# Optimization experiments

Measured on AMD Instinct MI355X. Metric: run time of the kernel, lower is better.

## Reference

```python
import jax, jax.numpy as jnp
import numpy as np

B, C, H, W = 8, 256, 96, 96
NQ, NCLS = 100, 12
OBJ_CH = NCLS - 2 + 1  # 11
EPS = 1e-6


def conv2d(x, w, b, pad):
    out = jax.lax.conv_general_dilated(x, w, (1, 1), [(pad, pad), (pad, pad)],
                                       dimension_numbers=('NCHW', 'OIHW', 'NCHW'))
    return out + b[None, :, None, None]


def conv1d(x, w, b):
    out = jax.lax.conv_general_dilated(x, w, (1,), [(0, 0)],
                                       dimension_numbers=('NCH', 'OIH', 'NCH'))
    return out + b[None, :, None]


def adaptive_avg_pool_1d(x, out_size):
    # x: [..., L]; torch AdaptiveAvgPool semantics: bin i = mean(x[floor(i*L/o):ceil((i+1)*L/o)])
    L = x.shape[-1]
    i = np.arange(out_size)
    starts = (i * L) // out_size
    ends = -((-(i + 1) * L) // out_size)
    csum = jnp.concatenate([jnp.zeros(x.shape[:-1] + (1,), x.dtype), jnp.cumsum(x, -1)], -1)
    sizes = jnp.asarray((ends - starts).astype(np.float32))
    return (csum[..., ends] - csum[..., starts]) / sizes


def local_max(p):
    # 8-neighbor local maximum with zero padding, thresholded at EPS
    pd = jnp.pad(p, ((0, 0), (0, 0), (1, 1), (1, 1)))
    m = ((p >= pd[:, :, :-2, 1:-1]) & (p >= pd[:, :, 2:, 1:-1]) &
         (p >= pd[:, :, 1:-1, :-2]) & (p >= pd[:, :, 1:-1, 2:]) &
         (p >= pd[:, :, :-2, :-2]) & (p >= pd[:, :, :-2, 2:]) &
         (p >= pd[:, :, 2:, :-2]) & (p >= pd[:, :, 2:, 2:]) & (p >= EPS))
    return m.astype(p.dtype)


def mask_and_nms(probs):
    # one-hot mask from argmax over foreground channels, then add local-max map
    oh = jax.nn.one_hot(jnp.argmax(probs[:, :-1], axis=1), probs.shape[1], axis=1, dtype=probs.dtype)
    p = probs * oh
    return p + local_max(p)


def head(x, w1, b1, w2, b2):
    return conv2d(jax.nn.relu(conv2d(x, w1, b1, 1)), w2, b2, 0)


def setup_inputs() -> dict:
    key = jax.random.key(0)
    ks = jax.random.split(key, 20)
    rn = lambda k, s: jax.random.normal(k, s, jnp.float32) * 0.02
    z = lambda n: jnp.zeros((n,), jnp.float32)
    return {
        'x': jax.random.normal(ks[0], (B, C, H, W), jnp.float32),
        'y': jax.random.normal(ks[1], (B, C, H, W), jnp.float32),
        'pos_embeddings': jax.random.normal(ks[2], (1, C, H, W), jnp.float32),
        'lw1': rn(ks[3], (C, C, 3, 3)), 'lb1': z(C),
        'lw2': rn(ks[4], (2, C, 1, 1)), 'lb2': z(2),
        'rw1': rn(ks[5], (C, C, 3, 3)), 'rb1': z(C),
        'rw2': rn(ks[6], (2, C, 1, 1)), 'rb2': z(2),
        'ow1': rn(ks[7], (C, C, 3, 3)), 'ob1': z(C),
        'ow2': rn(ks[8], (OBJ_CH, C, 1, 1)), 'ob2': z(OBJ_CH),
        'cw1': rn(ks[9], (64, C, 3, 3)), 'cb1': z(64),
        'cw2': rn(ks[10], (32, 64, 3, 3)), 'cb2': z(32),
        'cm_lw': rn(ks[11], (778 * 2, 778 * 32)), 'cm_lb': z(778 * 2),
        'c1d_w': rn(ks[12], (C, 2, 3)), 'c1d_b': z(C),
        'q_lw': rn(ks[13], (NQ * C, C)), 'q_lb': z(NQ * C),
    }


def reference(x, y, pos_embeddings, lw1, lb1, lw2, lb2, rw1, rb1, rw2, rb2,
              ow1, ob1, ow2, ob2, cw1, cb1, cw2, cb2, cm_lw, cm_lb,
              c1d_w, c1d_b, q_lw, q_lb):
    b = x.shape[0]
    left_logits = head(x, lw1, lb1, lw2, lb2)
    right_logits = head(x, rw1, rb1, rw2, rb2)
    obj_logits = head(x, ow1, ob1, ow2, ob2)

    left_p = mask_and_nms(jax.nn.softmax(left_logits, axis=1))
    right_p = mask_and_nms(jax.nn.softmax(right_logits, axis=1))
    obj_p = mask_and_nms(jax.nn.softmax(obj_logits, axis=1))

    hw = H * W
    idx_l = jax.lax.top_k(left_p[:, 0].reshape(b, hw), 40)[1]
    idx_r = jax.lax.top_k(right_p[:, 0].reshape(b, hw), 40)[1]
    idx_o = jax.lax.top_k(obj_p[:, :-1].reshape(b, OBJ_CH - 1, hw).max(axis=1), 20)[1]
    idx = jnp.concatenate([idx_l, idx_r, idx_o], axis=1)  # [B, 100]

    xf = x.reshape(b, C, hw)
    topk_proposals = jnp.take_along_axis(xf, jnp.broadcast_to(idx[:, None, :], (b, C, NQ)), axis=2)
    pf = jnp.broadcast_to(pos_embeddings, (b, C, H, W)).reshape(b, C, hw)
    topk_pos = jnp.take_along_axis(pf, jnp.broadcast_to(idx[:, None, :], (b, C, NQ)), axis=2)

    # contact map estimation branch
    h = jax.nn.relu(conv2d(y, cw1, cb1, 1))
    h = jax.nn.relu(conv2d(h, cw2, cb2, 1))  # [B,32,H,W]
    h = jnp.mean(h, axis=3)                  # adaptive pool width -> 1
    h = adaptive_avg_pool_1d(h, 778)         # [B,32,778]
    cm = h.reshape(b, -1) @ cm_lw.T + cm_lb  # [B,1556]
    contact_map = cm.reshape(b, 2, 778, 1)

    # ContactMapConvolution
    cc = conv1d(contact_map.reshape(b, 2, 778), c1d_w, c1d_b)  # [B,C,776]
    cc = jnp.mean(cc, axis=2)                                  # [B,C]
    feat = (cc @ q_lw.T + q_lb).reshape(b, C, NQ)              # [B,C,100]

    topk_proposals = topk_proposals + feat
    return (topk_proposals, topk_pos, left_logits, right_logits, obj_logits, contact_map)
```

## Files before the change

### kernel.cpp

```cpp
#include <hip/hip_runtime.h>
#include <float.h>
#include <math.h>

#define B_ 8
#define C_ 256
#define H_ 96
#define W_ 96
#define HW_ 9216
#define NQ_ 100
#define EPS_ 1e-6f
#define PADW_ 98
#define PADIMG_ 9604
#define PALLOC_ 76880

typedef unsigned short ushort_t;
typedef __attribute__((ext_vector_type(8))) short bf16x8;
typedef __attribute__((ext_vector_type(16))) float f32x16;

typedef __attribute__((address_space(3))) unsigned int as3_u32;
typedef __attribute__((address_space(1))) unsigned int as1_u32;

__device__ __forceinline__ void gl16(const void* g, void* l) {
    __builtin_amdgcn_global_load_lds(
        (const as1_u32*)(unsigned long long)g,
        (as3_u32*)(unsigned int)(unsigned long long)l, 16, 0, 0);
}

__device__ __forceinline__ ushort_t bf16_of(float v) {
    unsigned u = __float_as_uint(v);
    u += 0x7fffu + ((u >> 16) & 1u);
    return (ushort_t)(u >> 16);
}
__device__ __forceinline__ float f_of_bf16(ushort_t h) {
    return __uint_as_float((unsigned)h << 16);
}

__global__ __launch_bounds__(256)
void zero_border_kernel(ushort_t* __restrict__ bh, ushort_t* __restrict__ bl, int Cch)
{
    int per = 388 * Cch / 8;
    int id = blockIdx.x * 256 + threadIdx.x;
    if (id >= 8 * per) return;
    int b = id / per, i = id - b * per;
    int pi = (i * 8) / Cch, c8 = (i * 8) % Cch;
    int yy, xx;
    if (pi < 98)      { yy = 0;            xx = pi; }
    else if (pi < 196){ yy = 97;           xx = pi - 98; }
    else if (pi < 292){ yy = pi - 195;     xx = 0; }
    else              { yy = pi - 291;     xx = 97; }
    size_t base = ((size_t)b * PADIMG_ + yy * PADW_ + xx) * Cch + c8;
    *(bf16x8*)&bh[base] = (bf16x8)(short)0;
    *(bf16x8*)&bl[base] = (bf16x8)(short)0;
}

__global__ __launch_bounds__(256)
void tsplit_kernel(const float* __restrict__ in, ushort_t* __restrict__ oh,
                   ushort_t* __restrict__ ol, int Cch)
{
    __shared__ float T[32][33];
    const int tx = threadIdx.x & 31, ty = threadIdx.x >> 5;
    const int p0 = blockIdx.x * 32, ci0 = blockIdx.y * 32, b = blockIdx.z;
#pragma unroll
    for (int i = 0; i < 4; ++i)
        T[ty + 8*i][tx] = in[((size_t)b*Cch + ci0 + ty + 8*i)*HW_ + p0 + tx];
    __syncthreads();
    const int y = p0 / 96, x0 = p0 - y * 96;
    const size_t Pp = (size_t)b*PADIMG_ + (size_t)(y + 1)*PADW_ + x0 + 1;
#pragma unroll
    for (int i = 0; i < 4; ++i) {
        float v = T[tx][ty + 8*i];
        ushort_t hi = bf16_of(v);
        float lo = v - f_of_bf16(hi);
        size_t o = (Pp + ty + 8*i)*Cch + ci0 + tx;
        oh[o] = hi;
        ol[o] = bf16_of(lo);
    }
}

__global__ __launch_bounds__(256)
void repack_kernel(const float* __restrict__ w, ushort_t* __restrict__ wh,
                   ushort_t* __restrict__ wl, int Cout, int Cin)
{
    int id = blockIdx.x*256 + threadIdx.x;
    int tot = 9*Cout*Cin;
    if (id >= tot) return;
    int tap = id / (Cout*Cin);
    int r = id - tap*(Cout*Cin);
    int oc = r / Cin, ci = r - oc*Cin;
    float v = w[((size_t)oc*Cin + ci)*9 + tap];
    ushort_t hi = bf16_of(v);
    wh[id] = hi;
    wl[id] = bf16_of(v - f_of_bf16(hi));
}

template<int WM, int WN, int MFR, int NFR, int CIN, int MODE, int KK, int BWAVES>
__global__ __launch_bounds__(WM*WN*64, (WM*WN + 3) / 4)
void conv_gemm_kernel(const ushort_t* __restrict__ Agh, const ushort_t* __restrict__ Agl,
                      const ushort_t* __restrict__ Wgh, const ushort_t* __restrict__ Wgl,
                      const float* __restrict__ bias1,
                      const float* __restrict__ w2, const float* __restrict__ b2,
                      float* __restrict__ out_logits,
                      ushort_t* __restrict__ Oth, ushort_t* __restrict__ Otl,
                      float* __restrict__ outf)
{
    constexpr int NW    = WM*WN;
    constexpr int NT    = NW*64;
    constexpr int BM    = WM*MFR*32;
    constexpr int COUT  = WN*NFR*32;
    constexpr int NG    = CIN/16;
    constexpr int NSTEP = NG*9;
    constexpr int APAD  = 512;
    constexpr int ASZ   = 2*APAD*16;
    constexpr int BSZ   = 2*COUT*16;
    constexpr int AROUNDS = 32;
    constexpr int BROUNDS = COUT/16;
    constexpr int AWAVES = NW - BWAVES;
    constexpr int AR_PER = AROUNDS/AWAVES;
    constexpr int BR_PER = BROUNDS/BWAVES;
    static_assert(BM == 288, "BM must be 288");
    static_assert(AROUNDS % AWAVES == 0, "");
    static_assert(BROUNDS % BWAVES == 0, "");

    __shared__ __align__(16) ushort_t ALds[2*ASZ];
    __shared__ __align__(16) ushort_t BLds[3*BSZ];

    const int tid  = threadIdx.x;
    const int lane = tid & 63;
    const int wid  = __builtin_amdgcn_readfirstlane(tid >> 6);
    const int wm   = wid / WN, wn = wid % WN;
    const int l31  = lane & 31, hh2 = lane >> 5;
    const int wnb  = wn * NFR * 32;

    const int cpx = gridDim.x >> 3;
    const int bid = (blockIdx.x & 7)*cpx + (blockIdx.x >> 3);
    const int bidx = bid >> 5;
    const int br   = bid & 31;
    const size_t S = (size_t)bidx*PADIMG_ + (size_t)(3*br)*PADW_;

    auto stageA = [&](int g, int sel) {
        ushort_t* dst = ALds + sel*ASZ;
        const int aw = wid - BWAVES;
#pragma unroll
        for (int j = 0; j < AR_PER; ++j) {
            int c = aw*AR_PER + j;
            int id = c*64 + lane;
            int split = id >> 10;
            int r2 = id & 1023;
            int pix = r2 >> 1, ch = r2 & 1;
            int ch2 = ch ^ (pix & 1);
            const ushort_t* src = (split ? Agl : Agh) + (S + pix)*CIN + g*16 + ch2*8;
            gl16(src, dst + (size_t)c*512);
        }
    };
    auto stageB = [&](int g, int tap, int sel) {
        ushort_t* dst = BLds + sel*BSZ;
#pragma unroll
        for (int j = 0; j < BR_PER; ++j) {
            int c = wid*BR_PER + j;
            int id = c*64 + lane;
            int split = id / (COUT*2);
            int r2 = id % (COUT*2);
            int row = r2 >> 1, ch = r2 & 1;
            int ch2 = ch ^ (row & 1);
            const ushort_t* src = (split ? Wgl : Wgh)
                + ((size_t)tap*COUT + row)*CIN + g*16 + ch2*8;
            gl16(src, dst + (size_t)c*512);
        }
    };

    f32x16 acc[MFR][NFR];
#pragma unroll
    for (int i = 0; i < MFR; ++i)
#pragma unroll
        for (int j = 0; j < NFR; ++j)
#pragma unroll
            for (int r = 0; r < 16; ++r) acc[i][j][r] = 0.f;

    if (wid < BWAVES) { stageB(0, 0, 0); stageB(0, 1, 1); }
    else stageA(0, 0);
    asm volatile("s_waitcnt vmcnt(0)" ::: "memory");
    __builtin_amdgcn_s_barrier();
    __builtin_amdgcn_sched_barrier(0);

    int g = 0, tap = 0;
#pragma unroll 1
    for (int step = 0; step < NSTEP; ++step) {
        __builtin_amdgcn_sched_barrier(0);
        if (wid < BWAVES) {
            if (step >= NSTEP - 1) asm volatile("s_waitcnt vmcnt(0)" ::: "memory");
            else                   asm volatile("s_waitcnt vmcnt(%0)" :: "n"(BR_PER) : "memory");
        } else if (tap == 0) {
            asm volatile("s_waitcnt vmcnt(0)" ::: "memory");
        }
        __builtin_amdgcn_s_barrier();
        __builtin_amdgcn_sched_barrier(0);

        if (wid < BWAVES) {
            if (step + 2 < NSTEP) {
                int t2 = tap + 2, g2 = g;
                if (t2 >= 9) { t2 -= 9; ++g2; }
                stageB(g2, t2, (step + 2) % 3);
            }
        } else if (tap == 0 && g + 1 < NG) {
            stageA(g + 1, (g + 1) & 1);
        }

        const int abase = (g & 1) * ASZ;
        const int bbase = (step % 3) * BSZ;
        const int dy = tap / 3, dx = tap - dy*3;
        const int tapoff = dy*PADW_ + dx;

        bf16x8 bh[NFR], bl[NFR];
#pragma unroll
        for (int nf = 0; nf < NFR; ++nf) {
            int n = wnb + nf*32 + l31;
            int o = bbase + n*16 + ((hh2 ^ (n & 1)) << 3);
            bh[nf] = *(const bf16x8*)&BLds[o];
            bl[nf] = *(const bf16x8*)&BLds[o + COUT*16];
        }
        __builtin_amdgcn_s_setprio(1);
#pragma unroll
        for (int mf = 0; mf < MFR; ++mf) {
            int row = wm*PADW_ + tapoff + mf*32 + l31;
            int o = abase + row*16 + ((hh2 ^ (row & 1)) << 3);
            bf16x8 ah = *(const bf16x8*)&ALds[o];
            bf16x8 al = *(const bf16x8*)&ALds[o + APAD*16];
#pragma unroll
            for (int nf = 0; nf < NFR; ++nf) {
                acc[mf][nf] = __builtin_amdgcn_mfma_f32_32x32x16_bf16(
                    ah, bh[nf], acc[mf][nf], 0, 0, 0);
                acc[mf][nf] = __builtin_amdgcn_mfma_f32_32x32x16_bf16(
                    al, bh[nf], acc[mf][nf], 0, 0, 0);
                acc[mf][nf] = __builtin_amdgcn_mfma_f32_32x32x16_bf16(
                    ah, bl[nf], acc[mf][nf], 0, 0, 0);
            }
        }
        __builtin_amdgcn_s_setprio(0);

        if (++tap == 9) { tap = 0; ++g; }
    }
    __syncthreads();

    float biasv[NFR];
#pragma unroll
    for (int nf = 0; nf < NFR; ++nf) biasv[nf] = bias1[wnb + nf*32 + l31];

    if constexpr (MODE == 0) {
        float* Lacc = (float*)ALds;
        float w2v[NFR][KK];
#pragma unroll
        for (int nf = 0; nf < NFR; ++nf)
#pragma unroll
            for (int k = 0; k < KK; ++k)
                w2v[nf][k] = w2[(size_t)k*COUT + wnb + nf*32 + l31];

#pragma unroll
        for (int mf = 0; mf < MFR; ++mf) {
#pragma unroll
            for (int r = 0; r < 16; ++r) {
                float v[KK];
#pragma unroll
                for (int k = 0; k < KK; ++k) v[k] = 0.f;
#pragma unroll
                for (int nf = 0; nf < NFR; ++nf) {
                    float rr = fmaxf(acc[mf][nf][r] + biasv[nf], 0.f);
#pragma unroll
                    for (int k = 0; k < KK; ++k) v[k] += rr * w2v[nf][k];
                }
#pragma unroll
                for (int k = 0; k < KK; ++k) {
                    v[k] += __shfl_xor(v[k], 1);
                    v[k] += __shfl_xor(v[k], 2);
                    v[k] += __shfl_xor(v[k], 4);
                    v[k] += __shfl_xor(v[k], 8);
                    v[k] += __shfl_xor(v[k], 16);
                }
                if (l31 == 0) {
                    int crow = (r & 3) + 8*(r >> 2) + 4*hh2;
                    int mrow = wm*96 + mf*32 + crow;
#pragma unroll
                    for (int k = 0; k < KK; ++k)
                        Lacc[((size_t)wn*BM + mrow)*KK + k] = v[k];
                }
            }
        }
        __syncthreads();
        for (int i = tid; i < BM*KK; i += NT) {
            int mrow = i / KK, k = i - mrow*KK;
            float s = b2[k];
#pragma unroll
            for (int w = 0; w < WN; ++w) s += Lacc[((size_t)w*BM + mrow)*KK + k];
            out_logits[((size_t)bidx*KK + k)*HW_ + br*288 + mrow] = s;
        }
    } else if constexpr (MODE == 1) {
#pragma unroll
        for (int mf = 0; mf < MFR; ++mf)
#pragma unroll
            for (int nf = 0; nf < NFR; ++nf)
#pragma unroll
                for (int r = 0; r < 16; ++r) {
                    float rr = fmaxf(acc[mf][nf][r] + biasv[nf], 0.f);
                    ushort_t hi = bf16_of(rr);
                    float lo = rr - f_of_bf16(hi);
                    int crow = (r & 3) + 8*(r >> 2) + 4*hh2;
                    int xx = mf*32 + crow;
                    size_t Pp = (size_t)bidx*PADIMG_
                              + (size_t)(3*br + wm + 1)*PADW_ + xx + 1;
                    size_t o = Pp*COUT + wnb + nf*32 + l31;
                    Oth[o] = hi;
                    Otl[o] = bf16_of(lo);
                }
    } else {
        float (*T)[BM + 1] = (float(*)[BM + 1])ALds;
#pragma unroll
        for (int mf = 0; mf < MFR; ++mf)
#pragma unroll
            for (int r = 0; r < 16; ++r) {
                float rr = fmaxf(acc[mf][0][r] + biasv[0], 0.f);
                int crow = (r & 3) + 8*(r >> 2) + 4*hh2;
                T[l31][wm*96 + mf*32 + crow] = rr;
            }
        __syncthreads();
        for (int i = tid; i < COUT*BM; i += NT) {
            int c = i / BM, m = i - c*BM;
            outf[((size_t)bidx*COUT + c)*HW_ + br*288 + m] = T[c][m];
        }
    }
}

__global__ __launch_bounds__(256)
void prob2_kernel(const float* __restrict__ logits, float* __restrict__ p0)
{
    int i = blockIdx.x * 256 + threadIdx.x;
    if (i >= B_ * HW_) return;
    int b = i / HW_, pix = i - b * HW_;
    float l0 = logits[(size_t)b * 2 * HW_ + pix];
    float l1 = logits[(size_t)b * 2 * HW_ + HW_ + pix];
    float m = fmaxf(l0, l1);
    float e0 = expf(l0 - m), e1 = expf(l1 - m);
    p0[i] = e0 / (e0 + e1);
}

__global__ __launch_bounds__(256)
void score2_kernel(const float* __restrict__ p, float* __restrict__ sc)
{
    int i = blockIdx.x * 256 + threadIdx.x;
    if (i >= B_ * HW_) return;
    int pix = i % HW_;
    int yy = pix / W_, xx = pix - (pix / W_) * W_;
    float c = p[i];
    bool ok = (c >= EPS_);
    const float* pb = p + (i - pix);
#pragma unroll
    for (int dy = -1; dy <= 1; ++dy)
#pragma unroll
        for (int dx = -1; dx <= 1; ++dx) {
            if (dy == 0 && dx == 0) continue;
            int ny = yy + dy, nx = xx + dx;
            float v = 0.f;
            if (ny >= 0 && ny < H_ && nx >= 0 && nx < W_) v = pb[ny * W_ + nx];
            ok = ok && (c >= v);
        }
    sc[i] = c + (ok ? 1.f : 0.f);
}

__global__ __launch_bounds__(256)
void probobj_kernel(const float* __restrict__ logits, float* __restrict__ pval,
                    int* __restrict__ cstar)
{
    int i = blockIdx.x * 256 + threadIdx.x;
    if (i >= B_ * HW_) return;
    int b = i / HW_, pix = i - b * HW_;
    const float* lb = logits + (size_t)b * 11 * HW_ + pix;
    float l[11];
#pragma unroll
    for (int c2 = 0; c2 < 11; ++c2) l[c2] = lb[(size_t)c2 * HW_];
    float m = l[0];
#pragma unroll
    for (int c2 = 1; c2 < 11; ++c2) m = fmaxf(m, l[c2]);
    float sum = 0.f;
#pragma unroll
    for (int c2 = 0; c2 < 11; ++c2) sum += expf(l[c2] - m);
    int a = 0; float bestl = l[0];
#pragma unroll
    for (int c2 = 1; c2 < 10; ++c2)
        if (l[c2] > bestl) { bestl = l[c2]; a = c2; }
    pval[i] = expf(bestl - m) / sum;
    cstar[i] = a;
}

__global__ __launch_bounds__(256)
void score11_kernel(const float* __restrict__ p, const int* __restrict__ cs,
                    float* __restrict__ sc)
{
    int i = blockIdx.x * 256 + threadIdx.x;
    if (i >= B_ * HW_) return;
    int pix = i % HW_;
    int yy = pix / W_, xx = pix - (pix / W_) * W_;
    float c = p[i];
    int cc = cs[i];
    bool ok = (c >= EPS_);
    int base = i - pix;
#pragma unroll
    for (int dy = -1; dy <= 1; ++dy)
#pragma unroll
        for (int dx = -1; dx <= 1; ++dx) {
            if (dy == 0 && dx == 0) continue;
            int ny = yy + dy, nx = xx + dx;
            float v = 0.f;
            if (ny >= 0 && ny < H_ && nx >= 0 && nx < W_) {
                int n = base + ny * W_ + nx;
                v = (cs[n] == cc) ? p[n] : 0.f;
            }
            ok = ok && (c >= v);
        }
    sc[i] = c + (ok ? 1.f : 0.f);
}

__global__ __launch_bounds__(256)
void topk_kernel(const float* __restrict__ scL, const float* __restrict__ scR,
                 const float* __restrict__ scO, int* __restrict__ idx)
{
    __shared__ float sv[HW_];
    __shared__ float rv[256];
    __shared__ int   ri[256];
    const int h = blockIdx.x, b = blockIdx.y;
    const float* src = (h == 0) ? scL : (h == 1) ? scR : scO;
    const int k = (h == 2) ? 20 : 40;
    const int off = b * NQ_ + ((h == 0) ? 0 : (h == 1) ? 40 : 80);

    for (int t = threadIdx.x; t < HW_; t += 256) sv[t] = src[(size_t)b * HW_ + t];
    __syncthreads();

    for (int kk = 0; kk < k; ++kk) {
        float bestv = -FLT_MAX; int besti = HW_;
        for (int t = threadIdx.x; t < HW_; t += 256) {
            float v = sv[t];
            if (v > bestv) { bestv = v; besti = t; }
        }
        rv[threadIdx.x] = bestv; ri[threadIdx.x] = besti;
        __syncthreads();
        for (int s = 128; s > 0; s >>= 1) {
            if (threadIdx.x < s) {
                float v2 = rv[threadIdx.x + s]; int i2 = ri[threadIdx.x + s];
                if (v2 > rv[threadIdx.x] ||
                    (v2 == rv[threadIdx.x] && i2 < ri[threadIdx.x])) {
                    rv[threadIdx.x] = v2; ri[threadIdx.x] = i2;
                }
            }
            __syncthreads();
        }
        if (threadIdx.x == 0) { idx[off + kk] = ri[0]; sv[ri[0]] = -FLT_MAX; }
        __syncthreads();
    }
}

__global__ __launch_bounds__(128)
void pool_kernel(const float* __restrict__ h2, float* __restrict__ pooled)
{
    int bc = blockIdx.x;
    __shared__ float row[96];
    for (int hh = threadIdx.x; hh < 96; hh += 128) {
        const float* p = h2 + (size_t)bc * HW_ + hh * W_;
        float s = 0.f;
        for (int ww = 0; ww < 96; ++ww) s += p[ww];
        row[hh] = s * (1.f / 96.f);
    }
    __syncthreads();
    for (int i = threadIdx.x; i < 778; i += 128) {
        int s0 = (i * 96) / 778;
        int e0 = ((i + 1) * 96 + 777) / 778;
        float s = 0.f;
        for (int t = s0; t < e0; ++t) s += row[t];
        pooled[(size_t)bc * 778 + i] = s / (float)(e0 - s0);
    }
}

__global__ __launch_bounds__(256)
void cm_kernel(const float* __restrict__ pooled, const float* __restrict__ cm_lw,
               const float* __restrict__ cm_lb, float* __restrict__ out5)
{
    const int j = blockIdx.x;
    const float* wr = cm_lw + (size_t)j * 24896;
    float acc[8];
#pragma unroll
    for (int b = 0; b < 8; ++b) acc[b] = 0.f;
    for (int t = threadIdx.x; t < 24896; t += 256) {
        float w = wr[t];
#pragma unroll
        for (int b = 0; b < 8; ++b) acc[b] += w * pooled[(size_t)b * 24896 + t];
    }
    __shared__ float red[8][256];
#pragma unroll
    for (int b = 0; b < 8; ++b) red[b][threadIdx.x] = acc[b];
    __syncthreads();
    for (int s = 128; s > 0; s >>= 1) {
        if (threadIdx.x < s) {
#pragma unroll
            for (int b = 0; b < 8; ++b) red[b][threadIdx.x] += red[b][threadIdx.x + s];
        }
        __syncthreads();
    }
    if (threadIdx.x < 8)
        out5[(size_t)threadIdx.x * 1556 + j] = red[threadIdx.x][0] + cm_lb[j];
}

__global__ __launch_bounds__(256)
void c1d_kernel(const float* __restrict__ cmap, const float* __restrict__ w,
                const float* __restrict__ bias, float* __restrict__ ccmean)
{
    int b = blockIdx.x;
    __shared__ float r[2][778];
    __shared__ float T[2][3];
    for (int t = threadIdx.x; t < 1556; t += 256)
        r[t / 778][t % 778] = cmap[(size_t)b * 1556 + t];
    __syncthreads();
    if (threadIdx.x < 2) {
        int ic = threadIdx.x;
        float s = 0.f;
        for (int i2 = 0; i2 < 778; ++i2) s += r[ic][i2];
        T[ic][0] = s - r[ic][776] - r[ic][777];
        T[ic][1] = s - r[ic][0]   - r[ic][777];
        T[ic][2] = s - r[ic][0]   - r[ic][1];
    }
    __syncthreads();
    int oc = threadIdx.x;
    float a = 0.f;
#pragma unroll
    for (int ic = 0; ic < 2; ++ic)
#pragma unroll
        for (int k = 0; k < 3; ++k)
            a += w[oc * 6 + ic * 3 + k] * T[ic][k];
    ccmean[b * 256 + oc] = a / 776.f + bias[oc];
}

__global__ __launch_bounds__(256)
void feat_kernel(const float* __restrict__ ccmean, const float* __restrict__ q_lw,
                 const float* __restrict__ q_lb, float* __restrict__ feat)
{
    __shared__ float cc[8][256];
    for (int t = threadIdx.x; t < 2048; t += 256) cc[t >> 8][t & 255] = ccmean[t];
    __syncthreads();
    int j = blockIdx.x * 256 + threadIdx.x;
    const float* wr = q_lw + (size_t)j * 256;
    float acc[8];
#pragma unroll
    for (int b = 0; b < 8; ++b) acc[b] = 0.f;
    for (int c = 0; c < 256; ++c) {
        float wv = wr[c];
#pragma unroll
        for (int b = 0; b < 8; ++b) acc[b] += wv * cc[b][c];
    }
    float qb = q_lb[j];
#pragma unroll
    for (int b = 0; b < 8; ++b) feat[(size_t)b * 25600 + j] = acc[b] + qb;
}

__global__ __launch_bounds__(256)
void gather_kernel(const float* __restrict__ x, const float* __restrict__ pos,
                   const float* __restrict__ feat, const int* __restrict__ idx,
                   float* __restrict__ out0, float* __restrict__ out1)
{
    int t = blockIdx.x * 256 + threadIdx.x;
    if (t >= B_ * C_ * NQ_) return;
    int q = t % NQ_;
    int c2 = (t / NQ_) % C_;
    int b = t / (C_ * NQ_);
    int p = idx[b * NQ_ + q];
    out0[t] = x[((size_t)b * C_ + c2) * HW_ + p] + feat[(size_t)b * 25600 + c2 * NQ_ + q];
    out1[t] = pos[(size_t)c2 * HW_ + p];
}

extern "C" void kernel_launch(void* const* d_in, const int* in_sizes, int n_in,
                              void* d_out, int out_size, void* d_ws, size_t ws_size,
                              hipStream_t stream) {
    const float* x    = (const float*)d_in[0];
    const float* y    = (const float*)d_in[1];
    const float* pos  = (const float*)d_in[2];
    const float* lw1  = (const float*)d_in[3];  const float* lb1 = (const float*)d_in[4];
    const float* lw2  = (const float*)d_in[5];  const float* lb2 = (const float*)d_in[6];
    const float* rw1  = (const float*)d_in[7];  const float* rb1 = (const float*)d_in[8];
    const float* rw2  = (const float*)d_in[9];  const float* rb2 = (const float*)d_in[10];
    const float* ow1  = (const float*)d_in[11]; const float* ob1 = (const float*)d_in[12];
    const float* ow2  = (const float*)d_in[13]; const float* ob2 = (const float*)d_in[14];
    const float* cw1  = (const float*)d_in[15]; const float* cb1 = (const float*)d_in[16];
    const float* cw2  = (const float*)d_in[17]; const float* cb2 = (const float*)d_in[18];
    const float* cmlw = (const float*)d_in[19]; const float* cmlb = (const float*)d_in[20];
    const float* c1dw = (const float*)d_in[21]; const float* c1db = (const float*)d_in[22];
    const float* qlw  = (const float*)d_in[23]; const float* qlb  = (const float*)d_in[24];

    float* out  = (float*)d_out;
    float* out0 = out;
    float* out1 = out + 204800;
    float* out2 = out + 409600;
    float* out3 = out + 557056;
    float* out4 = out + 704512;
    float* out5 = out + 1515520;

    float* ws = (float*)d_ws;
    ushort_t* Rh   = (ushort_t*)(ws);
    ushort_t* Rl   = (ushort_t*)(ws + 9840640);
    ushort_t* h1h  = (ushort_t*)(ws + 19681280);
    ushort_t* h1l  = (ushort_t*)(ws + 22141440);
    float*    h2   = ws + 24601600;
    ushort_t* wLh  = (ushort_t*)(ws + 26960896);
    ushort_t* wLl  = (ushort_t*)(ws + 27255808);
    ushort_t* wRh  = (ushort_t*)(ws + 27550720);
    ushort_t* wRl  = (ushort_t*)(ws + 27845632);
    ushort_t* wOh  = (ushort_t*)(ws + 28140544);
    ushort_t* wOl  = (ushort_t*)(ws + 28435456);
    ushort_t* wc1h = (ushort_t*)(ws + 28730368);
    ushort_t* wc1l = (ushort_t*)(ws + 28804096);
    ushort_t* wc2h = (ushort_t*)(ws + 28877824);
    ushort_t* wc2l = (ushort_t*)(ws + 28887040);
    float* pooled  = ws + 28896256;
    float* ccmean  = ws + 29095424;
    float* feat    = ws + 29097472;
    float* pmap    = ws + 29302272;
    int*   csmap   = (int*)(ws + 29376000);
    float* scL     = ws + 29449728;
    float* scR     = ws + 29523456;
    float* scO     = ws + 29597184;
    int*   idxb    = (int*)(ws + 29670912);
    (void)in_sizes; (void)n_in; (void)out_size; (void)ws_size; (void)pos;

    zero_border_kernel<<<388, 256, 0, stream>>>(Rh, Rl, 256);
    zero_border_kernel<<<97,  256, 0, stream>>>(h1h, h1l, 64);
    repack_kernel<<<(9*256*256+255)/256, 256, 0, stream>>>(lw1, wLh, wLl, 256, 256);
    repack_kernel<<<(9*256*256+255)/256, 256, 0, stream>>>(rw1, wRh, wRl, 256, 256);
    repack_kernel<<<(9*256*256+255)/256, 256, 0, stream>>>(ow1, wOh, wOl, 256, 256);
    repack_kernel<<<(9*64*256+255)/256,  256, 0, stream>>>(cw1, wc1h, wc1l, 64, 256);
    repack_kernel<<<(9*32*64+255)/256,   256, 0, stream>>>(cw2, wc2h, wc2l, 32, 64);

    tsplit_kernel<<<dim3(288, 8, 8), 256, 0, stream>>>(y, Rh, Rl, 256);
    conv_gemm_kernel<3,2,3,1,256,1,1,4><<<256, 384, 0, stream>>>(
        Rh, Rl, wc1h, wc1l, cb1, nullptr, nullptr, nullptr, h1h, h1l, nullptr);
    conv_gemm_kernel<3,1,3,1,64,2,1,2><<<256, 192, 0, stream>>>(
        h1h, h1l, wc2h, wc2l, cb2, nullptr, nullptr, nullptr, nullptr, nullptr, h2);
    pool_kernel<<<256, 128, 0, stream>>>(h2, pooled);
    cm_kernel<<<1556, 256, 0, stream>>>(pooled, cmlw, cmlb, out5);
    c1d_kernel<<<8, 256, 0, stream>>>(out5, c1dw, c1db, ccmean);
    feat_kernel<<<100, 256, 0, stream>>>(ccmean, qlw, qlb, feat);

    tsplit_kernel<<<dim3(288, 8, 8), 256, 0, stream>>>(x, Rh, Rl, 256);
    conv_gemm_kernel<3,4,3,2,256,0,2,8><<<256, 768, 0, stream>>>(
        Rh, Rl, wLh, wLl, lb1, lw2, lb2, out2, nullptr, nullptr, nullptr);
    conv_gemm_kernel<3,4,3,2,256,0,2,8><<<256, 768, 0, stream>>>(
        Rh, Rl, wRh, wRl, rb1, rw2, rb2, out3, nullptr, nullptr, nullptr);
    conv_gemm_kernel<3,4,3,2,256,0,11,8><<<256, 768, 0, stream>>>(
        Rh, Rl, wOh, wOl, ob1, ow2, ob2, out4, nullptr, nullptr, nullptr);

    prob2_kernel<<<288, 256, 0, stream>>>(out2, pmap);
    score2_kernel<<<288, 256, 0, stream>>>(pmap, scL);
    prob2_kernel<<<288, 256, 0, stream>>>(out3, pmap);
    score2_kernel<<<288, 256, 0, stream>>>(pmap, scR);
    probobj_kernel<<<288, 256, 0, stream>>>(out4, pmap, csmap);
    score11_kernel<<<288, 256, 0, stream>>>(pmap, csmap, scO);

    topk_kernel<<<dim3(3, 8), 256, 0, stream>>>(scL, scR, scO, idxb);
    gather_kernel<<<800, 256, 0, stream>>>(x, pos, feat, idxb, out0, out1);
}
```

Baseline: 1.176 ms.

## Software-pipeline B fragment loads with register double-buffering and one barrier per step

Restructures the conv GEMM main loop so the B fragments for the next step are read from LDS into a second register set while the current step's MFMAs run. The loop is unrolled by two to alternate register sets, prefetches three B stages ahead, and keeps a single barrier per step. The LDS XOR swizzle changes from row&1 to (row>>2)&1 to reduce bank conflicts, and the contact-branch kernels use fewer B-loading waves. This adds register pressure and depends on the changed wait counts being correct.

Result: slower. 1.289 ms (+9.6%).

```diff
diff --git a/kernel.cpp b/kernel.cpp
--- a/kernel.cpp
+++ b/kernel.cpp
@@ -120,6 +120,7 @@
     static_assert(BM == 288, "BM must be 288");
     static_assert(AROUNDS % AWAVES == 0, "");
     static_assert(BROUNDS % BWAVES == 0, "");
+    static_assert(NSTEP % 2 == 0, "");
 
     __shared__ __align__(16) ushort_t ALds[2*ASZ];
     __shared__ __align__(16) ushort_t BLds[3*BSZ];
@@ -146,9 +147,9 @@
             int id = c*64 + lane;
             int split = id >> 10;
             int r2 = id & 1023;
-            int pix = r2 >> 1, ch = r2 & 1;
-            int ch2 = ch ^ (pix & 1);
-            const ushort_t* src = (split ? Agl : Agh) + (S + pix)*CIN + g*16 + ch2*8;
+            int row = r2 >> 1, slot = r2 & 1;
+            int ch = slot ^ ((row >> 2) & 1);
+            const ushort_t* src = (split ? Agl : Agh) + (S + row)*CIN + g*16 + ch*8;
             gl16(src, dst + (size_t)c*512);
         }
     };
@@ -160,10 +161,10 @@
             int id = c*64 + lane;
             int split = id / (COUT*2);
             int r2 = id % (COUT*2);
-            int row = r2 >> 1, ch = r2 & 1;
-            int ch2 = ch ^ (row & 1);
+            int row = r2 >> 1, slot = r2 & 1;
+            int ch = slot ^ ((row >> 2) & 1);
             const ushort_t* src = (split ? Wgl : Wgh)
-                + ((size_t)tap*COUT + row)*CIN + g*16 + ch2*8;
+                + ((size_t)tap*COUT + row)*CIN + g*16 + ch*8;
             gl16(src, dst + (size_t)c*512);
         }
     };
@@ -176,69 +177,89 @@
 #pragma unroll
             for (int r = 0; r < 16; ++r) acc[i][j][r] = 0.f;
 
-    if (wid < BWAVES) { stageB(0, 0, 0); stageB(0, 1, 1); }
-    else stageA(0, 0);
-    asm volatile("s_waitcnt vmcnt(0)" ::: "memory");
+    bf16x8 bhX[NFR], blX[NFR], bhY[NFR], blY[NFR];
+
+    if (wid < BWAVES) {
+        stageB(0, 0, 0); stageB(0, 1, 1); stageB(0, 2, 2);
+        asm volatile("s_waitcnt vmcnt(%0)" :: "n"(BR_PER) : "memory");
+    } else {
+        stageA(0, 0);
+        asm volatile("s_waitcnt vmcnt(0)" ::: "memory");
+    }
     __builtin_amdgcn_s_barrier();
     __builtin_amdgcn_sched_barrier(0);
+#pragma unroll
+    for (int nf = 0; nf < NFR; ++nf) {
+        int n = wnb + nf*32 + l31;
+        int o = n*16 + ((hh2 ^ ((n >> 2) & 1)) << 3);
+        bhX[nf] = *(const bf16x8*)&BLds[o];
+        blX[nf] = *(const bf16x8*)&BLds[o + COUT*16];
+    }
+    asm volatile("s_waitcnt lgkmcnt(0)" ::: "memory");
+    __builtin_amdgcn_sched_barrier(0);
+    __builtin_amdgcn_s_barrier();
+    __builtin_amdgcn_sched_barrier(0);
+
+#define CONV_BODY(SS, GG, TT, BHC, BLC, BHN, BLN)                               \
+    {                                                                           \
+        if (wid < BWAVES) {                                                     \
+            int s3 = (SS) + 3;                                                  \
+            if (s3 < NSTEP) { int g3 = s3/9; stageB(g3, s3 - g3*9, s3 % 3); }   \
+        } else if ((TT) == 0 && (GG) + 1 < NG) {                                \
+            stageA((GG) + 1, ((GG) + 1) & 1);                                   \
+        }                                                                       \
+        const int abase = ((GG) & 1) * ASZ;                                     \
+        const int dyq = (TT)/3;                                                 \
+        const int tapoff = dyq*PADW_ + ((TT) - dyq*3);                          \
+        bf16x8 ah[MFR], al[MFR];                                                \
+        _Pragma("unroll")                                                       \
+        for (int mf = 0; mf < MFR; ++mf) {                                      \
+            int row = wm*PADW_ + tapoff + mf*32 + l31;                          \
+            int o = abase + row*16 + ((hh2 ^ ((row >> 2) & 1)) << 3);           \
+            ah[mf] = *(const bf16x8*)&ALds[o];                                  \
+            al[mf] = *(const bf16x8*)&ALds[o + APAD*16];                        \
+        }                                                                       \
+        const int bnbase = (((SS) + 1) % 3) * BSZ;                              \
+        _Pragma("unroll")                                                       \
+        for (int nf = 0; nf < NFR; ++nf) {                                      \
+            int n = wnb + nf*32 + l31;                                          \
+            int o = bnbase + n*16 + ((hh2 ^ ((n >> 2) & 1)) << 3);              \
+            BHN[nf] = *(const bf16x8*)&BLds[o];                                 \
+            BLN[nf] = *(const bf16x8*)&BLds[o + COUT*16];                       \
+        }                                                                       \
+        __builtin_amdgcn_s_setprio(1);                                          \
+        _Pragma("unroll")                                                       \
+        for (int mf = 0; mf < MFR; ++mf) {                                      \
+            _Pragma("unroll")                                                   \
+            for (int nf = 0; nf < NFR; ++nf) {                                  \
+                acc[mf][nf] = __builtin_amdgcn_mfma_f32_32x32x16_bf16(          \
+                    ah[mf], BHC[nf], acc[mf][nf], 0, 0, 0);                     \
+                acc[mf][nf] = __builtin_amdgcn_mfma_f32_32x32x16_bf16(          \
+                    al[mf], BHC[nf], acc[mf][nf], 0, 0, 0);                     \
+                acc[mf][nf] = __builtin_amdgcn_mfma_f32_32x32x16_bf16(          \
+                    ah[mf], BLC[nf], acc[mf][nf], 0, 0, 0);                     \
+            }                                                                   \
+        }                                                                       \
+        __builtin_amdgcn_s_setprio(0);                                          \
+        __builtin_amdgcn_sched_barrier(0);                                      \
+        asm volatile("s_waitcnt lgkmcnt(0)" ::: "memory");                      \
+        if (wid < BWAVES)                                                       \
+            asm volatile("s_waitcnt vmcnt(%0)" :: "n"(BR_PER) : "memory");      \
+        else if ((TT) == 8)                                                     \
+            asm volatile("s_waitcnt vmcnt(0)" ::: "memory");                    \
+        __builtin_amdgcn_s_barrier();                                           \
+        __builtin_amdgcn_sched_barrier(0);                                      \
+    }
 
     int g = 0, tap = 0;
 #pragma unroll 1
-    for (int step = 0; step < NSTEP; ++step) {
-        __builtin_amdgcn_sched_barrier(0);
-        if (wid < BWAVES) {
-            if (step >= NSTEP - 1) asm volatile("s_waitcnt vmcnt(0)" ::: "memory");
-            else                   asm volatile("s_waitcnt vmcnt(%0)" :: "n"(BR_PER) : "memory");
-        } else if (tap == 0) {
-            asm volatile("s_waitcnt vmcnt(0)" ::: "memory");
-        }
-        __builtin_amdgcn_s_barrier();
-        __builtin_amdgcn_sched_barrier(0);
-
-        if (wid < BWAVES) {
-            if (step + 2 < NSTEP) {
-                int t2 = tap + 2, g2 = g;
-                if (t2 >= 9) { t2 -= 9; ++g2; }
-                stageB(g2, t2, (step + 2) % 3);
-            }
-        } else if (tap == 0 && g + 1 < NG) {
-            stageA(g + 1, (g + 1) & 1);
-        }
-
-        const int abase = (g & 1) * ASZ;
-        const int bbase = (step % 3) * BSZ;
-        const int dy = tap / 3, dx = tap - dy*3;
-        const int tapoff = dy*PADW_ + dx;
-
-        bf16x8 bh[NFR], bl[NFR];
-#pragma unroll
-        for (int nf = 0; nf < NFR; ++nf) {
-            int n = wnb + nf*32 + l31;
-            int o = bbase + n*16 + ((hh2 ^ (n & 1)) << 3);
-            bh[nf] = *(const bf16x8*)&BLds[o];
-            bl[nf] = *(const bf16x8*)&BLds[o + COUT*16];
-        }
-        __builtin_amdgcn_s_setprio(1);
-#pragma unroll
-        for (int mf = 0; mf < MFR; ++mf) {
-            int row = wm*PADW_ + tapoff + mf*32 + l31;
-            int o = abase + row*16 + ((hh2 ^ (row & 1)) << 3);
-            bf16x8 ah = *(const bf16x8*)&ALds[o];
-            bf16x8 al = *(const bf16x8*)&ALds[o + APAD*16];
-#pragma unroll
-            for (int nf = 0; nf < NFR; ++nf) {
-                acc[mf][nf] = __builtin_amdgcn_mfma_f32_32x32x16_bf16(
-                    ah, bh[nf], acc[mf][nf], 0, 0, 0);
-                acc[mf][nf] = __builtin_amdgcn_mfma_f32_32x32x16_bf16(
-                    al, bh[nf], acc[mf][nf], 0, 0, 0);
-                acc[mf][nf] = __builtin_amdgcn_mfma_f32_32x32x16_bf16(
-                    ah, bl[nf], acc[mf][nf], 0, 0, 0);
-            }
-        }
-        __builtin_amdgcn_s_setprio(0);
-
-        if (++tap == 9) { tap = 0; ++g; }
-    }
+    for (int s = 0; s < NSTEP; s += 2) {
+        CONV_BODY(s,     g, tap, bhX, blX, bhY, blY);
+        ++tap; if (tap == 9) { tap = 0; ++g; }
+        CONV_BODY(s + 1, g, tap, bhY, blY, bhX, blX);
+        ++tap; if (tap == 9) { tap = 0; ++g; }
+    }
+#undef CONV_BODY
     __syncthreads();
 
     float biasv[NFR];
@@ -633,9 +654,9 @@
     repack_kernel<<<(9*32*64+255)/256,   256, 0, stream>>>(cw2, wc2h, wc2l, 32, 64);
 
     tsplit_kernel<<<dim3(288, 8, 8), 256, 0, stream>>>(y, Rh, Rl, 256);
-    conv_gemm_kernel<3,2,3,1,256,1,1,4><<<256, 384, 0, stream>>>(
+    conv_gemm_kernel<3,2,3,1,256,1,1,2><<<256, 384, 0, stream>>>(
         Rh, Rl, wc1h, wc1l, cb1, nullptr, nullptr, nullptr, h1h, h1l, nullptr);
-    conv_gemm_kernel<3,1,3,1,64,2,1,2><<<256, 192, 0, stream>>>(
+    conv_gemm_kernel<3,1,3,1,64,2,1,1><<<256, 192, 0, stream>>>(
         h1h, h1l, wc2h, wc2l, cb2, nullptr, nullptr, nullptr, nullptr, nullptr, h2);
     pool_kernel<<<256, 128, 0, stream>>>(h2, pooled);
     cm_kernel<<<1556, 256, 0, stream>>>(pooled, cmlw, cmlb, out5);
```

## Load conv weights directly to registers and unroll taps per channel group

Applied to the files above, without the earlier changes.

Drops the LDS staging of weight (B) tiles and the producer/consumer wave split. Every wave now loads its weight fragments straight from global memory into registers, two taps ahead, using a repacked weight layout that makes each fragment read contiguous. The nine taps are unrolled per channel group, so there is one barrier per group instead of one per tap, and the A-tile swizzle is changed. This cuts LDS traffic and barriers, but it adds register pressure and exposes global-load latency on the weight reads.

Result: no change. 1.182 ms (+0.5%).

```diff
diff --git a/kernel.cpp b/kernel.cpp
--- a/kernel.cpp
+++ b/kernel.cpp
@@ -85,15 +85,18 @@
     int tot = 9*Cout*Cin;
     if (id >= tot) return;
     int tap = id / (Cout*Cin);
-    int r = id - tap*(Cout*Cin);
-    int oc = r / Cin, ci = r - oc*Cin;
+    int r   = id - tap*(Cout*Cin);
+    int g   = r / (Cout*16);
+    int r2  = r - g*(Cout*16);
+    int oc  = r2 >> 4, cr = r2 & 15;
+    int ci  = g*16 + cr;
     float v = w[((size_t)oc*Cin + ci)*9 + tap];
     ushort_t hi = bf16_of(v);
     wh[id] = hi;
     wl[id] = bf16_of(v - f_of_bf16(hi));
 }
 
-template<int WM, int WN, int MFR, int NFR, int CIN, int MODE, int KK, int BWAVES>
+template<int WM, int WN, int MFR, int NFR, int CIN, int MODE, int KK>
 __global__ __launch_bounds__(WM*WN*64, (WM*WN + 3) / 4)
 void conv_gemm_kernel(const ushort_t* __restrict__ Agh, const ushort_t* __restrict__ Agl,
                       const ushort_t* __restrict__ Wgh, const ushort_t* __restrict__ Wgl,
@@ -108,21 +111,12 @@
     constexpr int BM    = WM*MFR*32;
     constexpr int COUT  = WN*NFR*32;
     constexpr int NG    = CIN/16;
-    constexpr int NSTEP = NG*9;
     constexpr int APAD  = 512;
     constexpr int ASZ   = 2*APAD*16;
-    constexpr int BSZ   = 2*COUT*16;
     constexpr int AROUNDS = 32;
-    constexpr int BROUNDS = COUT/16;
-    constexpr int AWAVES = NW - BWAVES;
-    constexpr int AR_PER = AROUNDS/AWAVES;
-    constexpr int BR_PER = BROUNDS/BWAVES;
     static_assert(BM == 288, "BM must be 288");
-    static_assert(AROUNDS % AWAVES == 0, "");
-    static_assert(BROUNDS % BWAVES == 0, "");
 
     __shared__ __align__(16) ushort_t ALds[2*ASZ];
-    __shared__ __align__(16) ushort_t BLds[3*BSZ];
 
     const int tid  = threadIdx.x;
     const int lane = tid & 63;
@@ -139,34 +133,17 @@
 
     auto stageA = [&](int g, int sel) {
         ushort_t* dst = ALds + sel*ASZ;
-        const int aw = wid - BWAVES;
-#pragma unroll
-        for (int j = 0; j < AR_PER; ++j) {
-            int c = aw*AR_PER + j;
+#pragma unroll 1
+        for (int c = wid; c < AROUNDS; c += NW) {
             int id = c*64 + lane;
             int split = id >> 10;
             int r2 = id & 1023;
-            int pix = r2 >> 1, ch = r2 & 1;
-            int ch2 = ch ^ (pix & 1);
-            const ushort_t* src = (split ? Agl : Agh) + (S + pix)*CIN + g*16 + ch2*8;
+            int row = r2 >> 1, slot = r2 & 1;
+            int ch = slot ^ ((row >> 2) & 1);
+            const ushort_t* src = (split ? Agl : Agh) + (S + row)*CIN + g*16 + ch*8;
             gl16(src, dst + (size_t)c*512);
         }
     };
-    auto stageB = [&](int g, int tap, int sel) {
-        ushort_t* dst = BLds + sel*BSZ;
-#pragma unroll
-        for (int j = 0; j < BR_PER; ++j) {
-            int c = wid*BR_PER + j;
-            int id = c*64 + lane;
-            int split = id / (COUT*2);
-            int r2 = id % (COUT*2);
-            int row = r2 >> 1, ch = r2 & 1;
-            int ch2 = ch ^ (row & 1);
-            const ushort_t* src = (split ? Wgl : Wgh)
-                + ((size_t)tap*COUT + row)*CIN + g*16 + ch2*8;
-            gl16(src, dst + (size_t)c*512);
-        }
-    };
 
     f32x16 acc[MFR][NFR];
 #pragma unroll
@@ -176,69 +153,70 @@
 #pragma unroll
             for (int r = 0; r < 16; ++r) acc[i][j][r] = 0.f;
 
-    if (wid < BWAVES) { stageB(0, 0, 0); stageB(0, 1, 1); }
-    else stageA(0, 0);
-    asm volatile("s_waitcnt vmcnt(0)" ::: "memory");
+    bf16x8 bh0[NFR], bl0[NFR], bh1[NFR], bl1[NFR], bh2[NFR], bl2[NFR];
+
+#define LOADB(G, T, BH, BL)                                                    \
+    {                                                                          \
+        _Pragma("unroll")                                                      \
+        for (int nf = 0; nf < NFR; ++nf) {                                     \
+            size_t o = ((size_t)((T)*NG + (G))*COUT + (wnb + nf*32 + l31))*16  \
+                       + hh2*8;                                                \
+            BH[nf] = *(const bf16x8*)&Wgh[o];                                  \
+            BL[nf] = *(const bf16x8*)&Wgl[o];                                  \
+        }                                                                      \
+    }
+
+    stageA(0, 0);
+    LOADB(0, 0, bh0, bl0);
+    LOADB(0, 1, bh1, bl1);
+    __builtin_amdgcn_sched_barrier(0);
+    asm volatile("s_waitcnt vmcnt(%0)" :: "n"(4*NFR) : "memory");
     __builtin_amdgcn_s_barrier();
     __builtin_amdgcn_sched_barrier(0);
 
-    int g = 0, tap = 0;
+#define TAPBODY(T, BHC, BLC, BHN, BLN)                                         \
+    {                                                                          \
+        if ((T) <= 6)            LOADB(g,     (T)+2, BHN, BLN)                 \
+        else if (g + 1 < NG)     LOADB(g+1,   (T)-7, BHN, BLN)                 \
+        const int tapoff = ((T)/3)*PADW_ + ((T) % 3);                          \
+        _Pragma("unroll")                                                      \
+        for (int mf = 0; mf < MFR; ++mf) {                                     \
+            int row = wm*PADW_ + tapoff + mf*32 + l31;                         \
+            int o = abase + row*16 + ((hh2 ^ ((row >> 2) & 1)) << 3);          \
+            bf16x8 ah = *(const bf16x8*)&ALds[o];                              \
+            bf16x8 al = *(const bf16x8*)&ALds[o + APAD*16];                    \
+            _Pragma("unroll")                                                  \
+            for (int nf = 0; nf < NFR; ++nf) {                                 \
+                acc[mf][nf] = __builtin_amdgcn_mfma_f32_32x32x16_bf16(         \
+                    ah, BHC[nf], acc[mf][nf], 0, 0, 0);                        \
+                acc[mf][nf] = __builtin_amdgcn_mfma_f32_32x32x16_bf16(         \
+                    al, BHC[nf], acc[mf][nf], 0, 0, 0);                        \
+                acc[mf][nf] = __builtin_amdgcn_mfma_f32_32x32x16_bf16(         \
+                    ah, BLC[nf], acc[mf][nf], 0, 0, 0);                        \
+            }                                                                  \
+        }                                                                      \
+    }
+
 #pragma unroll 1
-    for (int step = 0; step < NSTEP; ++step) {
+    for (int g = 0; g < NG; ++g) {
+        if (g + 1 < NG) stageA(g + 1, (g + 1) & 1);
+        const int abase = (g & 1) * ASZ;
+        TAPBODY(0, bh0, bl0, bh2, bl2);
+        TAPBODY(1, bh1, bl1, bh0, bl0);
+        TAPBODY(2, bh2, bl2, bh1, bl1);
+        TAPBODY(3, bh0, bl0, bh2, bl2);
+        TAPBODY(4, bh1, bl1, bh0, bl0);
+        TAPBODY(5, bh2, bl2, bh1, bl1);
+        TAPBODY(6, bh0, bl0, bh2, bl2);
+        TAPBODY(7, bh1, bl1, bh0, bl0);
+        TAPBODY(8, bh2, bl2, bh1, bl1);
         __builtin_amdgcn_sched_barrier(0);
-        if (wid < BWAVES) {
-            if (step >= NSTEP - 1) asm volatile("s_waitcnt vmcnt(0)" ::: "memory");
-            else                   asm volatile("s_waitcnt vmcnt(%0)" :: "n"(BR_PER) : "memory");
-        } else if (tap == 0) {
-            asm volatile("s_waitcnt vmcnt(0)" ::: "memory");
-        }
+        asm volatile("s_waitcnt vmcnt(%0)" :: "n"(4*NFR) : "memory");
         __builtin_amdgcn_s_barrier();
         __builtin_amdgcn_sched_barrier(0);
-
-        if (wid < BWAVES) {
-            if (step + 2 < NSTEP) {
-                int t2 = tap + 2, g2 = g;
-                if (t2 >= 9) { t2 -= 9; ++g2; }
-                stageB(g2, t2, (step + 2) % 3);
-            }
-        } else if (tap == 0 && g + 1 < NG) {
-            stageA(g + 1, (g + 1) & 1);
-        }
-
-        const int abase = (g & 1) * ASZ;
-        const int bbase = (step % 3) * BSZ;
-        const int dy = tap / 3, dx = tap - dy*3;
-        const int tapoff = dy*PADW_ + dx;
-
-        bf16x8 bh[NFR], bl[NFR];
-#pragma unroll
-        for (int nf = 0; nf < NFR; ++nf) {
-            int n = wnb + nf*32 + l31;
-            int o = bbase + n*16 + ((hh2 ^ (n & 1)) << 3);
-            bh[nf] = *(const bf16x8*)&BLds[o];
-            bl[nf] = *(const bf16x8*)&BLds[o + COUT*16];
-        }
-        __builtin_amdgcn_s_setprio(1);
-#pragma unroll
-        for (int mf = 0; mf < MFR; ++mf) {
-            int row = wm*PADW_ + tapoff + mf*32 + l31;
-            int o = abase + row*16 + ((hh2 ^ (row & 1)) << 3);
-            bf16x8 ah = *(const bf16x8*)&ALds[o];
-            bf16x8 al = *(const bf16x8*)&ALds[o + APAD*16];
-#pragma unroll
-            for (int nf = 0; nf < NFR; ++nf) {
-                acc[mf][nf] = __builtin_amdgcn_mfma_f32_32x32x16_bf16(
-                    ah, bh[nf], acc[mf][nf], 0, 0, 0);
-                acc[mf][nf] = __builtin_amdgcn_mfma_f32_32x32x16_bf16(
-                    al, bh[nf], acc[mf][nf], 0, 0, 0);
-                acc[mf][nf] = __builtin_amdgcn_mfma_f32_32x32x16_bf16(
-                    ah, bl[nf], acc[mf][nf], 0, 0, 0);
-            }
-        }
-        __builtin_amdgcn_s_setprio(0);
-
-        if (++tap == 9) { tap = 0; ++g; }
-    }
+    }
+#undef TAPBODY
+#undef LOADB
     __syncthreads();
 
     float biasv[NFR];
@@ -633,9 +611,9 @@
     repack_kernel<<<(9*32*64+255)/256,   256, 0, stream>>>(cw2, wc2h, wc2l, 32, 64);
 
     tsplit_kernel<<<dim3(288, 8, 8), 256, 0, stream>>>(y, Rh, Rl, 256);
-    conv_gemm_kernel<3,2,3,1,256,1,1,4><<<256, 384, 0, stream>>>(
+    conv_gemm_kernel<3,2,3,1,256,1,1><<<256, 384, 0, stream>>>(
         Rh, Rl, wc1h, wc1l, cb1, nullptr, nullptr, nullptr, h1h, h1l, nullptr);
-    conv_gemm_kernel<3,1,3,1,64,2,1,2><<<256, 192, 0, stream>>>(
+    conv_gemm_kernel<3,1,3,1,64,2,1><<<256, 192, 0, stream>>>(
         h1h, h1l, wc2h, wc2l, cb2, nullptr, nullptr, nullptr, nullptr, nullptr, h2);
     pool_kernel<<<256, 128, 0, stream>>>(h2, pooled);
     cm_kernel<<<1556, 256, 0, stream>>>(pooled, cmlw, cmlb, out5);
@@ -643,11 +621,11 @@
     feat_kernel<<<100, 256, 0, stream>>>(ccmean, qlw, qlb, feat);
 
     tsplit_kernel<<<dim3(288, 8, 8), 256, 0, stream>>>(x, Rh, Rl, 256);
-    conv_gemm_kernel<3,4,3,2,256,0,2,8><<<256, 768, 0, stream>>>(
+    conv_gemm_kernel<3,4,3,2,256,0,2><<<256, 768, 0, stream>>>(
         Rh, Rl, wLh, wLl, lb1, lw2, lb2, out2, nullptr, nullptr, nullptr);
-    conv_gemm_kernel<3,4,3,2,256,0,2,8><<<256, 768, 0, stream>>>(
+    conv_gemm_kernel<3,4,3,2,256,0,2><<<256, 768, 0, stream>>>(
         Rh, Rl, wRh, wRl, rb1, rw2, rb2, out3, nullptr, nullptr, nullptr);
-    conv_gemm_kernel<3,4,3,2,256,0,11,8><<<256, 768, 0, stream>>>(
+    conv_gemm_kernel<3,4,3,2,256,0,11><<<256, 768, 0, stream>>>(
         Rh, Rl, wOh, wOl, ob1, ow2, ob2, out4, nullptr, nullptr, nullptr);
 
     prob2_kernel<<<288, 256, 0, stream>>>(out2, pmap);
```
